# Optimization experiments

Hardware: AMD Instinct MI355X
Metric: run time of the kernel (lower is better)

Reference implementation:

```python
import jax, jax.numpy as jnp
import numpy as np

N_DET, N_T, NY, NX, B = 128, 2048, 256, 256, 4


def setup_inputs() -> dict:
    key = jax.random.key(0)
    k1, k2, k3 = jax.random.split(key, 3)
    sino = jax.random.normal(k1, (B, 1, N_DET, N_T), dtype=jnp.float32)
    # lut[..., 0]: fractional time-of-flight index in [0, n_t-1)
    tof = jax.random.uniform(k2, (NY, NX, N_DET), dtype=jnp.float32) * (N_T - 1)
    # lut[..., 1]: linear-interp fraction alpha in [0, 1)
    alpha = jax.random.uniform(k3, (NY, NX, N_DET), dtype=jnp.float32)
    lut = jnp.stack([tof, alpha], axis=-1)  # [ny, nx, n_det, 2]
    return {"sino": sino, "lut": lut}


def reference(sino, lut):
    b, _, n_det, n_t = sino.shape
    ny, nx = lut.shape[0], lut.shape[1]
    P = ny * nx

    # Precompute (as in __init__): floor index, validity mask, interp fraction.
    k_floor = jnp.floor(lut[..., 0])
    valid = (k_floor >= 0) & (k_floor < n_t - 1)
    k0 = jnp.clip(k_floor, 0, max(n_t - 2, 0)).astype(jnp.int32)  # [ny,nx,n_det]
    alpha = lut[..., 1]

    # Hann apodization window over detectors (non-trainable buffer).
    apod = (0.5 - 0.5 * jnp.cos(
        2.0 * jnp.pi * jnp.arange(n_det, dtype=jnp.float32) / max(n_det - 1, 1)
    )).astype(sino.dtype)

    S = sino[:, 0]  # [B, n_det, n_t]

    # Move detector axis first so we can gather all detectors at once.
    k0t = k0.reshape(P, n_det).T          # [n_det, P]
    at = alpha.reshape(P, n_det).T        # [n_det, P]
    vt = valid.reshape(P, n_det).T.astype(sino.dtype)  # [n_det, P]

    s0 = jnp.take_along_axis(S, k0t[None], axis=2)        # [B, n_det, P]
    s1 = jnp.take_along_axis(S, (k0t + 1)[None], axis=2)  # [B, n_det, P]
    sk = ((1.0 - at) * s0 + at * s1) * vt                  # masked lerp

    out = jnp.einsum('d,bdp->bp', apod, sk)                # apodized reduce over detectors
    norm = jnp.maximum(apod.sum(), jnp.finfo(apod.dtype).tiny)
    return (out / norm).reshape(b, 1, ny, nx)
```

## Files before the change

kernel.cpp:

```cpp
#include <hip/hip_runtime.h>
#include <hip/hip_fp16.h>

#define N_DET 128
#define N_T   2048
#define NPIX  65536
#define NBATCH 4

__global__ __launch_bounds__(256) void sino_pack_kernel(
    const float* __restrict__ sino, float4* __restrict__ wsT) {
  const int idx = blockIdx.x * blockDim.x + threadIdx.x;
  const int t = idx & (N_T - 1);
  const int idx1 = (t < N_T - 1) ? idx + 1 : idx;
  __half h[8];
#pragma unroll
  for (int b = 0; b < NBATCH; ++b) {
    h[b]     = __float2half(sino[b * N_DET * N_T + idx]);
    h[b + 4] = __float2half(sino[b * N_DET * N_T + idx1]);
  }
  wsT[idx] = *reinterpret_cast<const float4*>(h);
}

__global__ __launch_bounds__(256) void das_packed_kernel(
    const float* __restrict__ lut, const float4* __restrict__ S,
    float* __restrict__ out) {
  const int lane = threadIdx.x & 63;
  const int p = blockIdx.x * 4 + (threadIdx.x >> 6);

  const float4 lv =
      reinterpret_cast<const float4*>(lut + (size_t)p * 2 * N_DET)[lane];

  float acc0 = 0.f, acc1 = 0.f, acc2 = 0.f, acc3 = 0.f;
  float wsum = 0.f;

#pragma unroll
  for (int j = 0; j < 2; ++j) {
    const int d = 2 * lane + j;
    const float tof = j ? lv.z : lv.x;
    const float a   = j ? lv.w : lv.y;

    const float kf = floorf(tof);
    const bool valid = (kf >= 0.0f) && (kf < (float)(N_T - 1));
    const float kcl = fminf(fmaxf(kf, 0.0f), (float)(N_T - 2));
    const int k0 = (int)kcl;

    const float apd =
        0.5f - 0.5f * cosf(6.28318530717958647692f *
                           (1.0f / (float)(N_DET - 1)) * (float)d);
    wsum += apd;
    const float w = valid ? apd : 0.0f;
    const float om = 1.0f - a;

    const float4 v = S[(size_t)d * N_T + k0];
    const __half2* hp = reinterpret_cast<const __half2*>(&v);
    const float2 s0a = __half22float2(hp[0]);
    const float2 s0b = __half22float2(hp[1]);
    const float2 s1a = __half22float2(hp[2]);
    const float2 s1b = __half22float2(hp[3]);

    acc0 += w * (om * s0a.x + a * s1a.x);
    acc1 += w * (om * s0a.y + a * s1a.y);
    acc2 += w * (om * s0b.x + a * s1b.x);
    acc3 += w * (om * s0b.y + a * s1b.y);
  }

#pragma unroll
  for (int off = 32; off > 0; off >>= 1) {
    acc0 += __shfl_xor(acc0, off);
    acc1 += __shfl_xor(acc1, off);
    acc2 += __shfl_xor(acc2, off);
    acc3 += __shfl_xor(acc3, off);
    wsum += __shfl_xor(wsum, off);
  }

  if (lane == 0) {
    const float inv = 1.0f / fmaxf(wsum, 1.17549435e-38f);
    out[0 * NPIX + p] = acc0 * inv;
    out[1 * NPIX + p] = acc1 * inv;
    out[2 * NPIX + p] = acc2 * inv;
    out[3 * NPIX + p] = acc3 * inv;
  }
}

__global__ __launch_bounds__(256) void das_fallback_kernel(
    const float* __restrict__ lut, const float* __restrict__ S,
    float* __restrict__ out) {
  const int lane = threadIdx.x & 63;
  const int p = blockIdx.x * 4 + (threadIdx.x >> 6);

  const float4 lv =
      reinterpret_cast<const float4*>(lut + (size_t)p * 2 * N_DET)[lane];

  float acc0 = 0.f, acc1 = 0.f, acc2 = 0.f, acc3 = 0.f;
  float wsum = 0.f;

#pragma unroll
  for (int j = 0; j < 2; ++j) {
    const int d = 2 * lane + j;
    const float tof = j ? lv.z : lv.x;
    const float a   = j ? lv.w : lv.y;
    const float kf = floorf(tof);
    const bool valid = (kf >= 0.0f) && (kf < (float)(N_T - 1));
    const float kcl = fminf(fmaxf(kf, 0.0f), (float)(N_T - 2));
    const int k0 = (int)kcl;
    const float apd =
        0.5f - 0.5f * cosf(6.28318530717958647692f *
                           (1.0f / (float)(N_DET - 1)) * (float)d);
    wsum += apd;
    const float w = valid ? apd : 0.0f;
    const float om = 1.0f - a;
    const float* row = S + (size_t)d * N_T + k0;
    acc0 += w * (om * row[0 * N_DET * N_T] + a * row[0 * N_DET * N_T + 1]);
    acc1 += w * (om * row[1 * N_DET * N_T] + a * row[1 * N_DET * N_T + 1]);
    acc2 += w * (om * row[2 * N_DET * N_T] + a * row[2 * N_DET * N_T + 1]);
    acc3 += w * (om * row[3 * N_DET * N_T] + a * row[3 * N_DET * N_T + 1]);
  }

#pragma unroll
  for (int off = 32; off > 0; off >>= 1) {
    acc0 += __shfl_xor(acc0, off);
    acc1 += __shfl_xor(acc1, off);
    acc2 += __shfl_xor(acc2, off);
    acc3 += __shfl_xor(acc3, off);
    wsum += __shfl_xor(wsum, off);
  }

  if (lane == 0) {
    const float inv = 1.0f / fmaxf(wsum, 1.17549435e-38f);
    out[0 * NPIX + p] = acc0 * inv;
    out[1 * NPIX + p] = acc1 * inv;
    out[2 * NPIX + p] = acc2 * inv;
    out[3 * NPIX + p] = acc3 * inv;
  }
}

extern "C" void kernel_launch(void* const* d_in, const int* in_sizes, int n_in,
                              void* d_out, int out_size, void* d_ws, size_t ws_size,
                              hipStream_t stream) {
  const float* sino = (const float*)d_in[0];
  const float* lut  = (const float*)d_in[1];
  float* out = (float*)d_out;

  const size_t need = (size_t)N_DET * N_T * sizeof(float4);
  if (ws_size >= need) {
    float4* wsT = (float4*)d_ws;
    sino_pack_kernel<<<(N_DET * N_T) / 256, 256, 0, stream>>>(sino, wsT);
    das_packed_kernel<<<NPIX / 4, 256, 0, stream>>>(lut, wsT, out);
  } else {
    das_fallback_kernel<<<NPIX / 4, 256, 0, stream>>>(lut, sino, out);
  }
}
```

Baseline: 134.3 us.

## Halve packed sinogram workspace by dropping duplicated neighbor samples; add nontemporal hints

The packed workspace now stores only the four batch fp16 samples per (detector, time), 8 bytes each, instead of also duplicating the t+1 samples. The gather kernel reads 16 bytes at 8-byte alignment, which covers samples k0 and k0+1 together. This halves the workspace footprint, so the gathered data fits better in cache. Nontemporal loads and stores are also added for the LUT stream, the input sinogram and the output, to reduce cache pollution. The risk is that the unaligned 16-byte loads may split across cache lines or compile to narrower loads. The gather at k0 reads up to k0+1 at most N_T-1, so it stays in bounds.

```diff
diff --git a/kernel.cpp b/kernel.cpp
--- a/kernel.cpp
+++ b/kernel.cpp
@@ -6,28 +6,32 @@
 #define NPIX  65536
 #define NBATCH 4
 
+typedef float f4_t __attribute__((ext_vector_type(4)));
+typedef f4_t __attribute__((aligned(8))) f4a8_t;
+
 __global__ __launch_bounds__(256) void sino_pack_kernel(
-    const float* __restrict__ sino, float4* __restrict__ wsT) {
+    const float* __restrict__ sino, float2* __restrict__ ws) {
   const int idx = blockIdx.x * blockDim.x + threadIdx.x;
-  const int t = idx & (N_T - 1);
-  const int idx1 = (t < N_T - 1) ? idx + 1 : idx;
-  __half h[8];
-#pragma unroll
-  for (int b = 0; b < NBATCH; ++b) {
-    h[b]     = __float2half(sino[b * N_DET * N_T + idx]);
-    h[b + 4] = __float2half(sino[b * N_DET * N_T + idx1]);
-  }
-  wsT[idx] = *reinterpret_cast<const float4*>(h);
+  const __half2 lo = __floats2half2_rn(
+      __builtin_nontemporal_load(sino + 0 * N_DET * N_T + idx),
+      __builtin_nontemporal_load(sino + 1 * N_DET * N_T + idx));
+  const __half2 hi = __floats2half2_rn(
+      __builtin_nontemporal_load(sino + 2 * N_DET * N_T + idx),
+      __builtin_nontemporal_load(sino + 3 * N_DET * N_T + idx));
+  union { struct { __half2 a, b; } h; float2 f; } u;
+  u.h.a = lo;
+  u.h.b = hi;
+  ws[idx] = u.f;
 }
 
 __global__ __launch_bounds__(256) void das_packed_kernel(
-    const float* __restrict__ lut, const float4* __restrict__ S,
+    const float* __restrict__ lut, const unsigned char* __restrict__ S8,
     float* __restrict__ out) {
   const int lane = threadIdx.x & 63;
   const int p = blockIdx.x * 4 + (threadIdx.x >> 6);
 
-  const float4 lv =
-      reinterpret_cast<const float4*>(lut + (size_t)p * 2 * N_DET)[lane];
+  const f4_t lv = __builtin_nontemporal_load(
+      reinterpret_cast<const f4_t*>(lut + (size_t)p * 2 * N_DET) + lane);
 
   float acc0 = 0.f, acc1 = 0.f, acc2 = 0.f, acc3 = 0.f;
   float wsum = 0.f;
@@ -50,7 +54,8 @@
     const float w = valid ? apd : 0.0f;
     const float om = 1.0f - a;
 
-    const float4 v = S[(size_t)d * N_T + k0];
+    const f4a8_t v = *reinterpret_cast<const f4a8_t*>(
+        S8 + ((size_t)d * N_T + k0) * 8);
     const __half2* hp = reinterpret_cast<const __half2*>(&v);
     const float2 s0a = __half22float2(hp[0]);
     const float2 s0b = __half22float2(hp[1]);
@@ -74,10 +79,10 @@
 
   if (lane == 0) {
     const float inv = 1.0f / fmaxf(wsum, 1.17549435e-38f);
-    out[0 * NPIX + p] = acc0 * inv;
-    out[1 * NPIX + p] = acc1 * inv;
-    out[2 * NPIX + p] = acc2 * inv;
-    out[3 * NPIX + p] = acc3 * inv;
+    __builtin_nontemporal_store(acc0 * inv, out + 0 * NPIX + p);
+    __builtin_nontemporal_store(acc1 * inv, out + 1 * NPIX + p);
+    __builtin_nontemporal_store(acc2 * inv, out + 2 * NPIX + p);
+    __builtin_nontemporal_store(acc3 * inv, out + 3 * NPIX + p);
   }
 }
 
@@ -140,11 +145,12 @@
   const float* lut  = (const float*)d_in[1];
   float* out = (float*)d_out;
 
-  const size_t need = (size_t)N_DET * N_T * sizeof(float4);
+  const size_t need = (size_t)N_DET * N_T * 8;
   if (ws_size >= need) {
-    float4* wsT = (float4*)d_ws;
-    sino_pack_kernel<<<(N_DET * N_T) / 256, 256, 0, stream>>>(sino, wsT);
-    das_packed_kernel<<<NPIX / 4, 256, 0, stream>>>(lut, wsT, out);
+    float2* ws = (float2*)d_ws;
+    sino_pack_kernel<<<(N_DET * N_T) / 256, 256, 0, stream>>>(sino, ws);
+    das_packed_kernel<<<NPIX / 4, 256, 0, stream>>>(
+        lut, (const unsigned char*)d_ws, out);
   } else {
     das_fallback_kernel<<<NPIX / 4, 256, 0, stream>>>(lut, sino, out);
   }
```

Result: slower. 141.2 us (+5.2%).
